# Optimization experiments

Hardware: AMD Instinct MI355X
Metric: run time of the kernel (lower is better)

## Reference

```python
import jax, jax.numpy as jnp
import numpy as np
from jax import lax

SK_ITERS = 32  # fixed number of morphological thinning steps (covers structures up to ~64px thick)


def _pool(x, op, init):
    # 3x3 'square' structuring element over [B, H, W]
    return lax.reduce_window(x, init, op, (1, 3, 3), (1, 1, 1), 'SAME')


def dilate(x):
    return _pool(x, lax.max, -jnp.inf)


def erode(x):
    return _pool(x, lax.min, jnp.inf)


def skeletonize(a):
    # Lantuejoul morphological skeleton with fixed iteration count (jit-friendly
    # stand-in for skimage Lee skeletonization + per-component CCL loop).
    # a: [B, H, W] binary float mask.
    def body(i, carry):
        e, s = carry
        opened = dilate(erode(e))
        s = jnp.maximum(s, e - opened)
        return erode(e), s

    _, s = lax.fori_loop(0, SK_ITERS, body, (a, jnp.zeros_like(a)))
    return s


def setup_inputs() -> dict:
    key = jax.random.key(0)
    k1, k2 = jax.random.split(key)
    pred = jax.random.normal(k1, (16, 2, 1024, 1024), dtype=jnp.float32)
    target = jax.random.randint(k2, (16, 1, 1024, 1024), 0, 2, dtype=jnp.int64)
    return {"pred": pred, "target": target, "epoch_num": 10}


def reference(pred, target, epoch_num):
    tgt = target[:, 0]                      # [B, H, W] int
    a = tgt.astype(pred.dtype)              # binary mask
    B, H, W = a.shape

    # foreground skeleton + dilated background skeleton (calc_back_skelen)
    fore_sk = skeletonize(a)
    back_sk = dilate(skeletonize(1.0 - a))

    # epoch-gated skeleton-aware pixel weight map (SkeletonAwareWeight)
    factor = jnp.minimum(jnp.asarray(epoch_num, pred.dtype) / 50.0, 1.0)
    w_map = 1.0 + factor * (fore_sk + back_sk)   # [B, H, W]

    # per-sample class weights: counts / min(counts); cw = sum(cw) - cw
    counts = jnp.stack([(tgt == 0).sum(axis=(1, 2)),
                        (tgt == 1).sum(axis=(1, 2))], axis=1).astype(pred.dtype)  # [B, 2]
    cw = counts / jnp.min(counts, axis=1, keepdims=True)
    cw = jnp.sum(cw, axis=1, keepdims=True) - cw                                   # [B, 2]
    cw_map = jnp.take_along_axis(cw, tgt.reshape(B, -1), axis=1).reshape(B, H, W)

    # weighted cross-entropy (WeightMapBortLoss core)
    logp = jax.nn.log_softmax(pred, axis=1)                       # [B, 2, H, W]
    ce = -jnp.take_along_axis(logp, tgt[:, None], axis=1)[:, 0]   # [B, H, W]
    return jnp.mean(w_map * cw_map * ce)
```

## Files before the change

### kernel.cpp

```cpp
#include <hip/hip_runtime.h>
#include <stdint.h>

typedef unsigned long long u64;
typedef unsigned int u32;
typedef unsigned short u16;

#define WPR 16
#define WORDS_PER_IMG (1024*WPR)
#define PIXELS_PER_IMG (1024*1024)
#define HALO 33
#define OWN 64
#define BROWS (OWN + 2*HALO)

__global__ __launch_bounds__(256) void k_pack(const int* __restrict__ tgt,
                                              u64* __restrict__ bits,
                                              u32* __restrict__ cpart) {
    __shared__ u16 marr[256];
    __shared__ u32 ws_[4];
    int t = threadIdx.x;
    const int4* p4 = (const int4*)(tgt + ((size_t)blockIdx.x * 256 + t) * 16);
    u32 m16 = 0;
    #pragma unroll
    for (int k = 0; k < 4; ++k) {
        int4 v = p4[k];
        m16 |= (u32)(v.x & 1) << (4 * k + 0);
        m16 |= (u32)(v.y & 1) << (4 * k + 1);
        m16 |= (u32)(v.z & 1) << (4 * k + 2);
        m16 |= (u32)(v.w & 1) << (4 * k + 3);
    }
    marr[t] = (u16)m16;
    u32 cnt = __popc(m16);
    for (int off = 32; off; off >>= 1) cnt += __shfl_down(cnt, off, 64);
    if ((t & 63) == 0) ws_[t >> 6] = cnt;
    __syncthreads();
    if (t < 64)
        bits[(size_t)blockIdx.x * 64 + t] = ((const u64*)marr)[t];
    if (t == 0) cpart[blockIdx.x] = ws_[0] + ws_[1] + ws_[2] + ws_[3];
}

__global__ __launch_bounds__(256) void k_skel(const u64* __restrict__ bits,
                                              u64* __restrict__ fore,
                                              u64* __restrict__ back) {
    __shared__ u64 bufs[3][BROWS][WPR];
    __shared__ int nz;
    int bid   = blockIdx.x;
    int strip = bid & 15;
    int task  = bid >> 4;
    int batch = task >> 1;
    int pol   = task & 1;
    int r0    = strip * OWN - HALO;
    const u64* img = bits + batch * WORDS_PER_IMG;

    u64 (*E)[WPR]  = bufs[0];
    u64 (*T1)[WPR] = bufs[1];
    u64 (*T2)[WPR] = bufs[2];

    int t = threadIdx.x;
    for (int idx = t; idx < BROWS * WPR; idx += 256) {
        int br = idx >> 4, w = idx & 15;
        int y = r0 + br;
        u64 v;
        if ((unsigned)y < 1024u) { v = img[(y << 4) + w]; if (pol) v = ~v; }
        else v = ~0ull;
        E[br][w] = v;
    }
    u64 s0 = 0, s1 = 0, s2 = 0, s3 = 0;
    __syncthreads();

    for (int k = 0; k < 32; ++k) {
        if (t == 0) nz = 0;
        for (int idx = t; idx < BROWS * WPR; idx += 256) {
            int br = idx >> 4, w = idx & 15;
            u64 c = E[br][w];
            u64 l = w ? E[br][w - 1] : ~0ull;
            u64 r = (w < 15) ? E[br][w + 1] : ~0ull;
            T1[br][w] = c & ((c << 1) | (l >> 63)) & ((c >> 1) | (r << 63));
        }
        __syncthreads();
        u64 anyv = 0;
        for (int idx = t; idx < BROWS * WPR; idx += 256) {
            int br = idx >> 4, w = idx & 15;
            int y  = r0 + br;
            u64 v = 0;
            if ((unsigned)y < 1024u) {
                u64 a_ = (br > 0 && (unsigned)(y - 1) < 1024u) ? T1[br - 1][w] : ~0ull;
                u64 b_ = T1[br][w];
                u64 c_ = (br < BROWS - 1 && (unsigned)(y + 1) < 1024u) ? T1[br + 1][w] : ~0ull;
                v = a_ & b_ & c_;
            }
            T2[br][w] = v;
            anyv |= v;
        }
        {
            u64 bal = __ballot(anyv != 0);
            if (bal && (t & 63) == 0) atomicOr(&nz, 1);
        }
        __syncthreads();
        if (nz == 0) {
            #pragma unroll
            for (int j = 0; j < 4; ++j) {
                int idx = t + j * 256;
                int br = HALO + (idx >> 4), w = idx & 15;
                u64 e = E[br][w];
                if (j == 0) s0 |= e; else if (j == 1) s1 |= e;
                else if (j == 2) s2 |= e; else s3 |= e;
            }
            break;
        }
        for (int idx = t; idx < BROWS * WPR; idx += 256) {
            int br = idx >> 4, w = idx & 15;
            u64 c = T2[br][w];
            u64 l = w ? T2[br][w - 1] : 0ull;
            u64 r = (w < 15) ? T2[br][w + 1] : 0ull;
            T1[br][w] = c | (c << 1) | (l >> 63) | (c >> 1) | (r << 63);
        }
        __syncthreads();
        #pragma unroll
        for (int j = 0; j < 4; ++j) {
            int idx = t + j * 256;
            int br = HALO + (idx >> 4), w = idx & 15;
            int y  = r0 + br;
            u64 a_ = ((unsigned)(y - 1) < 1024u) ? T1[br - 1][w] : 0ull;
            u64 b_ = T1[br][w];
            u64 c_ = ((unsigned)(y + 1) < 1024u) ? T1[br + 1][w] : 0ull;
            u64 add = E[br][w] & ~(a_ | b_ | c_);
            if (j == 0) s0 |= add; else if (j == 1) s1 |= add;
            else if (j == 2) s2 |= add; else s3 |= add;
        }
        u64 (*tmp)[WPR] = E; E = T2; T2 = tmp;
        __syncthreads();
    }

    u64* plane = (pol ? back : fore) + batch * WORDS_PER_IMG;
    #pragma unroll
    for (int j = 0; j < 4; ++j) {
        int idx = t + j * 256;
        int yo = strip * OWN + (idx >> 4);
        int w  = idx & 15;
        u64 sv = (j == 0) ? s0 : (j == 1) ? s1 : (j == 2) ? s2 : s3;
        plane[(yo << 4) + w] = sv;
    }
}

__global__ __launch_bounds__(256) void k_loss(const float* __restrict__ pred,
                                              const u64* __restrict__ bits,
                                              const u64* __restrict__ fore,
                                              const u64* __restrict__ back,
                                              const u32* __restrict__ cpart,
                                              const int* __restrict__ epochp,
                                              float* __restrict__ partials) {
    const float LOG2E = 1.4426950408889634f;
    const float LN2   = 0.6931471805599453f;

    int b = blockIdx.x >> 9;

    __shared__ u32 cs[4];
    __shared__ float s_c1;
    {
        u32 v = cpart[(b << 8) + threadIdx.x];
        for (int off = 32; off; off >>= 1) v += __shfl_down(v, off, 64);
        if ((threadIdx.x & 63) == 0) cs[threadIdx.x >> 6] = v;
        __syncthreads();
        if (threadIdx.x == 0) s_c1 = (float)(cs[0] + cs[1] + cs[2] + cs[3]);
        __syncthreads();
    }

    int tid = blockIdx.x * 256 + threadIdx.x;
    int p   = tid << 3;
    int rem = p & (PIXELS_PER_IMG - 1);
    int y   = rem >> 10;
    int x   = rem & 1023;

    const float* pb = pred + (size_t)b * (2 * PIXELS_PER_IMG);
    const float* r0p = pb + (y << 10) + x;
    const float* r1p = pb + PIXELS_PER_IMG + (y << 10) + x;
    float4 q0a = *(const float4*)(r0p);
    float4 q0b = *(const float4*)(r0p + 4);
    float4 q1a = *(const float4*)(r1p);
    float4 q1b = *(const float4*)(r1p + 4);

    int w  = x >> 6;
    int wi = (b << 14) + (y << 4) + w;
    u64 tw = bits[wi];
    u64 fw = fore[wi];

    const u64* bb = back + (b << 14);
    int rbase = y << 4;
    u64 m0 = bb[rbase + w];
    u64 mL = w ? bb[rbase + w - 1] : 0ull;
    u64 mR = (w < 15) ? bb[rbase + w + 1] : 0ull;
    if (y > 0) {
        m0 |= bb[rbase - 16 + w];
        if (w) mL |= bb[rbase - 16 + w - 1];
        if (w < 15) mR |= bb[rbase - 16 + w + 1];
    }
    if (y < 1023) {
        m0 |= bb[rbase + 16 + w];
        if (w) mL |= bb[rbase + 16 + w - 1];
        if (w < 15) mR |= bb[rbase + 16 + w + 1];
    }
    u64 dil = m0 | (m0 << 1) | (mL >> 63) | (m0 >> 1) | (mR << 63);

    float c1 = s_c1;
    float c0 = (float)PIXELS_PER_IMG - c1;
    float mn = fminf(c0, c1);
    float rmn = __builtin_amdgcn_rcpf(mn);
    float w0 = c1 * rmn, w1 = c0 * rmn;
    float factor = fminf((float)epochp[0] / 50.0f, 1.0f);

    int j0 = x & 63;
    u32 t8 = (u32)(tw  >> j0) & 255u;
    u32 f8 = (u32)(fw  >> j0) & 255u;
    u32 b8 = (u32)(dil >> j0) & 255u;

    float p0v[8] = {q0a.x, q0a.y, q0a.z, q0a.w, q0b.x, q0b.y, q0b.z, q0b.w};
    float p1v[8] = {q1a.x, q1a.y, q1a.z, q1a.w, q1b.x, q1b.y, q1b.z, q1b.w};

    float acc = 0.f;
    #pragma unroll
    for (int i = 0; i < 8; ++i) {
        u32 tt = (t8 >> i) & 1u;
        float fb = (float)(((f8 >> i) & 1u) + ((b8 >> i) & 1u));
        float wmap = 1.0f + factor * fb;
        float cw = tt ? w1 : w0;
        float diff  = p1v[i] - p0v[i];
        float adiff = fabsf(diff);
        float T = LN2 * __builtin_amdgcn_logf(1.0f + __builtin_amdgcn_exp2f(-adiff * LOG2E));
        float ce = fmaf(tt ? -0.5f : 0.5f, diff, fmaf(0.5f, adiff, T));
        acc = fmaf(wmap * cw, ce, acc);
    }
    for (int off = 32; off; off >>= 1) acc += __shfl_down(acc, off, 64);
    __shared__ float wsum[4];
    if ((threadIdx.x & 63) == 0) wsum[threadIdx.x >> 6] = acc;
    __syncthreads();
    if (threadIdx.x == 0)
        partials[blockIdx.x] = wsum[0] + wsum[1] + wsum[2] + wsum[3];
}

__global__ __launch_bounds__(256) void k_reduce(const float* __restrict__ partials,
                                                float* __restrict__ out) {
    double acc = 0.0;
    for (int i = threadIdx.x; i < 8192; i += 256) acc += (double)partials[i];
    for (int off = 32; off; off >>= 1) acc += __shfl_down(acc, off, 64);
    __shared__ double sd[4];
    if ((threadIdx.x & 63) == 0) sd[threadIdx.x >> 6] = acc;
    __syncthreads();
    if (threadIdx.x == 0)
        out[0] = (float)((sd[0] + sd[1] + sd[2] + sd[3]) / 16777216.0);
}

extern "C" void kernel_launch(void* const* d_in, const int* in_sizes, int n_in,
                              void* d_out, int out_size, void* d_ws, size_t ws_size,
                              hipStream_t stream) {
    const float* pred   = (const float*)d_in[0];
    const int*   target = (const int*)d_in[1];
    const int*   epoch  = (const int*)d_in[2];

    char* ws = (char*)d_ws;
    u32*   cpart    = (u32*)(ws + 1024);
    float* partials = (float*)(ws + (1u << 17));
    u64*   bits     = (u64*)(ws + (1u << 20));
    u64*   fore     = (u64*)(ws + (3u << 20));
    u64*   back     = (u64*)(ws + (5u << 20));

    hipLaunchKernelGGL(k_pack,   dim3(4096), dim3(256), 0, stream, target, bits, cpart);
    hipLaunchKernelGGL(k_skel,   dim3(512),  dim3(256), 0, stream, bits, fore, back);
    hipLaunchKernelGGL(k_loss,   dim3(8192), dim3(256), 0, stream, pred, bits, fore, back,
                       cpart, epoch, partials);
    hipLaunchKernelGGL(k_reduce, dim3(1),    dim3(256), 0, stream, partials, (float*)d_out);
}
```

Baseline: 66.21 us.

## Register-window fused erosion in skeleton kernel and shared-memory bit staging in loss

The skeleton kernel now maps one row-half (8 words) to each thread and computes the full 3x3 erosion and the opening's dilation from three-row register windows. The separate horizontal and vertical shared-memory passes are gone, which cuts each iteration to two buffers and two barriers, with a padded row stride. Strips are re-cut to 66 owned rows with a 31-row halo. The loss kernel loads each block's two rows of target, fore and back bit-words into shared memory and computes the back dilation once per word instead of once per thread. The reduced halo and the new strip geometry carry a boundary-correctness risk.

After: 58.40 us. 1.13x faster.

```diff
diff --git a/kernel.cpp b/kernel.cpp
--- a/kernel.cpp
+++ b/kernel.cpp
@@ -8,9 +8,11 @@
 #define WPR 16
 #define WORDS_PER_IMG (1024*WPR)
 #define PIXELS_PER_IMG (1024*1024)
-#define HALO 33
-#define OWN 64
-#define BROWS (OWN + 2*HALO)
+
+#define SOWN 66
+#define SHALO 31
+#define SROWS 128
+#define SPAD 17
 
 __global__ __launch_bounds__(256) void k_pack(const int* __restrict__ tgt,
                                               u64* __restrict__ bits,
@@ -41,105 +43,108 @@
 __global__ __launch_bounds__(256) void k_skel(const u64* __restrict__ bits,
                                               u64* __restrict__ fore,
                                               u64* __restrict__ back) {
-    __shared__ u64 bufs[3][BROWS][WPR];
-    __shared__ int nz;
+    __shared__ u64 bufA[SROWS][SPAD];
+    __shared__ u64 bufB[SROWS][SPAD];
+    __shared__ int nzbuf[2];
+
     int bid   = blockIdx.x;
     int strip = bid & 15;
     int task  = bid >> 4;
     int batch = task >> 1;
     int pol   = task & 1;
-    int r0    = strip * OWN - HALO;
+    int r0    = strip * SOWN - SHALO;
     const u64* img = bits + batch * WORDS_PER_IMG;
 
-    u64 (*E)[WPR]  = bufs[0];
-    u64 (*T1)[WPR] = bufs[1];
-    u64 (*T2)[WPR] = bufs[2];
-
-    int t = threadIdx.x;
-    for (int idx = t; idx < BROWS * WPR; idx += 256) {
-        int br = idx >> 4, w = idx & 15;
-        int y = r0 + br;
-        u64 v;
-        if ((unsigned)y < 1024u) { v = img[(y << 4) + w]; if (pol) v = ~v; }
-        else v = ~0ull;
-        E[br][w] = v;
-    }
-    u64 s0 = 0, s1 = 0, s2 = 0, s3 = 0;
-    __syncthreads();
-
-    for (int k = 0; k < 32; ++k) {
-        if (t == 0) nz = 0;
-        for (int idx = t; idx < BROWS * WPR; idx += 256) {
-            int br = idx >> 4, w = idx & 15;
-            u64 c = E[br][w];
-            u64 l = w ? E[br][w - 1] : ~0ull;
-            u64 r = (w < 15) ? E[br][w + 1] : ~0ull;
-            T1[br][w] = c & ((c << 1) | (l >> 63)) & ((c >> 1) | (r << 63));
-        }
+    int t  = threadIdx.x;
+    int r  = t >> 1;
+    int h  = t & 1;
+    int w0 = h << 3;
+    int y  = r0 + r;
+    bool yok   = ((unsigned)y < 1024u);
+    bool owned = yok && (r >= SHALO) && (r < SHALO + SOWN);
+
+    u64 (*E)[SPAD]  = bufA;
+    u64 (*Er)[SPAD] = bufB;
+
+    if (yok) {
+        const u64* src = img + (y << 4) + w0;
+        #pragma unroll
+        for (int k = 0; k < 8; ++k) {
+            u64 v = src[k];
+            E[r][w0 + k] = pol ? ~v : v;
+        }
+    } else {
+        #pragma unroll
+        for (int k = 0; k < 8; ++k) E[r][w0 + k] = 0;
+    }
+    if (t < 2) nzbuf[t] = 0;
+
+    u64 s[8] = {0,0,0,0,0,0,0,0};
+    u64 corig[8];
+
+    auto ldwin = [&](u64 (*B)[SPAD], int rr, u64 oob, u64* d) {
+        int yy = r0 + rr;
+        if (rr >= 0 && rr < SROWS && (unsigned)yy < 1024u) {
+            d[0] = (w0 > 0) ? B[rr][w0 - 1] : oob;
+            #pragma unroll
+            for (int k = 0; k < 8; ++k) d[k + 1] = B[rr][w0 + k];
+            d[9] = (w0 + 8 < 16) ? B[rr][w0 + 8] : oob;
+        } else {
+            #pragma unroll
+            for (int k = 0; k < 10; ++k) d[k] = oob;
+        }
+    };
+    #define HOR_E(d, k) (d[k] & ((d[k] << 1) | (d[k-1] >> 63)) & ((d[k] >> 1) | (d[k+1] << 63)))
+    #define HOR_D(d, k) (d[k] | (d[k] << 1) | (d[k-1] >> 63) | (d[k] >> 1) | (d[k+1] << 63))
+
+    __syncthreads();
+    for (int it = 0; it < 32; ++it) {
+        u64 rm[10], rc[10], rp[10];
+        ldwin(E, r - 1, ~0ull, rm);
+        ldwin(E, r,     ~0ull, rc);
+        ldwin(E, r + 1, ~0ull, rp);
+        u64 any = 0;
+        #pragma unroll
+        for (int k = 0; k < 8; ++k) {
+            u64 v = HOR_E(rm, k + 1) & HOR_E(rc, k + 1) & HOR_E(rp, k + 1);
+            if (!yok) v = 0;
+            any |= v;
+            corig[k] = rc[k + 1];
+            Er[r][w0 + k] = v;
+        }
+        u64 bal = __ballot(any != 0);
+        if (bal && (t & 63) == 0) atomicOr(&nzbuf[it & 1], 1);
+        if (t == 0) nzbuf[(it + 1) & 1] = 0;
         __syncthreads();
-        u64 anyv = 0;
-        for (int idx = t; idx < BROWS * WPR; idx += 256) {
-            int br = idx >> 4, w = idx & 15;
-            int y  = r0 + br;
-            u64 v = 0;
-            if ((unsigned)y < 1024u) {
-                u64 a_ = (br > 0 && (unsigned)(y - 1) < 1024u) ? T1[br - 1][w] : ~0ull;
-                u64 b_ = T1[br][w];
-                u64 c_ = (br < BROWS - 1 && (unsigned)(y + 1) < 1024u) ? T1[br + 1][w] : ~0ull;
-                v = a_ & b_ & c_;
-            }
-            T2[br][w] = v;
-            anyv |= v;
-        }
-        {
-            u64 bal = __ballot(anyv != 0);
-            if (bal && (t & 63) == 0) atomicOr(&nz, 1);
-        }
-        __syncthreads();
-        if (nz == 0) {
-            #pragma unroll
-            for (int j = 0; j < 4; ++j) {
-                int idx = t + j * 256;
-                int br = HALO + (idx >> 4), w = idx & 15;
-                u64 e = E[br][w];
-                if (j == 0) s0 |= e; else if (j == 1) s1 |= e;
-                else if (j == 2) s2 |= e; else s3 |= e;
+        if (nzbuf[it & 1] == 0) {
+            if (owned) {
+                #pragma unroll
+                for (int k = 0; k < 8; ++k) s[k] |= corig[k];
             }
             break;
         }
-        for (int idx = t; idx < BROWS * WPR; idx += 256) {
-            int br = idx >> 4, w = idx & 15;
-            u64 c = T2[br][w];
-            u64 l = w ? T2[br][w - 1] : 0ull;
-            u64 r = (w < 15) ? T2[br][w + 1] : 0ull;
-            T1[br][w] = c | (c << 1) | (l >> 63) | (c >> 1) | (r << 63);
-        }
+        if (owned) {
+            u64 dm[10], dc[10], dp[10];
+            ldwin(Er, r - 1, 0ull, dm);
+            ldwin(Er, r,     0ull, dc);
+            ldwin(Er, r + 1, 0ull, dp);
+            #pragma unroll
+            for (int k = 0; k < 8; ++k) {
+                u64 op = HOR_D(dm, k + 1) | HOR_D(dc, k + 1) | HOR_D(dp, k + 1);
+                s[k] |= corig[k] & ~op;
+            }
+        }
+        { u64 (*tmp)[SPAD] = E; E = Er; Er = tmp; }
         __syncthreads();
-        #pragma unroll
-        for (int j = 0; j < 4; ++j) {
-            int idx = t + j * 256;
-            int br = HALO + (idx >> 4), w = idx & 15;
-            int y  = r0 + br;
-            u64 a_ = ((unsigned)(y - 1) < 1024u) ? T1[br - 1][w] : 0ull;
-            u64 b_ = T1[br][w];
-            u64 c_ = ((unsigned)(y + 1) < 1024u) ? T1[br + 1][w] : 0ull;
-            u64 add = E[br][w] & ~(a_ | b_ | c_);
-            if (j == 0) s0 |= add; else if (j == 1) s1 |= add;
-            else if (j == 2) s2 |= add; else s3 |= add;
-        }
-        u64 (*tmp)[WPR] = E; E = T2; T2 = tmp;
-        __syncthreads();
-    }
-
-    u64* plane = (pol ? back : fore) + batch * WORDS_PER_IMG;
-    #pragma unroll
-    for (int j = 0; j < 4; ++j) {
-        int idx = t + j * 256;
-        int yo = strip * OWN + (idx >> 4);
-        int w  = idx & 15;
-        u64 sv = (j == 0) ? s0 : (j == 1) ? s1 : (j == 2) ? s2 : s3;
-        plane[(yo << 4) + w] = sv;
-    }
+    }
+
+    if (owned) {
+        u64* plane = (pol ? back : fore) + batch * WORDS_PER_IMG + (y << 4) + w0;
+        #pragma unroll
+        for (int k = 0; k < 8; ++k) plane[k] = s[k];
+    }
+    #undef HOR_E
+    #undef HOR_D
 }
 
 __global__ __launch_bounds__(256) void k_loss(const float* __restrict__ pred,
@@ -152,26 +157,50 @@
     const float LOG2E = 1.4426950408889634f;
     const float LN2   = 0.6931471805599453f;
 
-    int b = blockIdx.x >> 9;
-
+    __shared__ u64 tb[2][16], tf[2][16], tbk[4][16], dil[2][16];
     __shared__ u32 cs[4];
     __shared__ float s_c1;
-    {
-        u32 v = cpart[(b << 8) + threadIdx.x];
-        for (int off = 32; off; off >>= 1) v += __shfl_down(v, off, 64);
-        if ((threadIdx.x & 63) == 0) cs[threadIdx.x >> 6] = v;
-        __syncthreads();
-        if (threadIdx.x == 0) s_c1 = (float)(cs[0] + cs[1] + cs[2] + cs[3]);
-        __syncthreads();
-    }
-
-    int tid = blockIdx.x * 256 + threadIdx.x;
-    int p   = tid << 3;
-    int rem = p & (PIXELS_PER_IMG - 1);
-    int y   = rem >> 10;
-    int x   = rem & 1023;
-
-    const float* pb = pred + (size_t)b * (2 * PIXELS_PER_IMG);
+    __shared__ float wsum[4];
+
+    int bid = blockIdx.x;
+    int b   = bid >> 9;
+    int rp  = bid & 511;
+    int y0  = rp << 1;
+    int t   = threadIdx.x;
+
+    u32 v = cpart[(b << 8) + t];
+    for (int off = 32; off; off >>= 1) v += __shfl_down(v, off, 64);
+    if ((t & 63) == 0) cs[t >> 6] = v;
+
+    int base = b << 14;
+    if (t < 32) {
+        int i = t >> 4, w = t & 15;
+        tb[i][w] = bits[base + ((y0 + i) << 4) + w];
+    } else if (t < 64) {
+        int tt = t - 32; int i = tt >> 4, w = tt & 15;
+        tf[i][w] = fore[base + ((y0 + i) << 4) + w];
+    } else if (t < 128) {
+        int tt = t - 64; int i = tt >> 4, w = tt & 15;
+        int yy = y0 - 1 + i;
+        tbk[i][w] = ((unsigned)yy < 1024u) ? back[base + (yy << 4) + w] : 0ull;
+    }
+    __syncthreads();
+    if (t < 32) {
+        int i = t >> 4, w = t & 15;
+        u64 m0 = tbk[i][w] | tbk[i + 1][w] | tbk[i + 2][w];
+        u64 mL = (w > 0)  ? (tbk[i][w - 1] | tbk[i + 1][w - 1] | tbk[i + 2][w - 1]) : 0ull;
+        u64 mR = (w < 15) ? (tbk[i][w + 1] | tbk[i + 1][w + 1] | tbk[i + 2][w + 1]) : 0ull;
+        dil[i][w] = m0 | (m0 << 1) | (mL >> 63) | (m0 >> 1) | (mR << 63);
+    }
+    if (t == 0) s_c1 = (float)(cs[0] + cs[1] + cs[2] + cs[3]);
+    __syncthreads();
+
+    int ry = t >> 7;
+    int xq = t & 127;
+    int x  = xq << 3;
+    int y  = y0 + ry;
+
+    const float* pb  = pred + (size_t)b * (2 * PIXELS_PER_IMG);
     const float* r0p = pb + (y << 10) + x;
     const float* r1p = pb + PIXELS_PER_IMG + (y << 10) + x;
     float4 q0a = *(const float4*)(r0p);
@@ -179,27 +208,10 @@
     float4 q1a = *(const float4*)(r1p);
     float4 q1b = *(const float4*)(r1p + 4);
 
-    int w  = x >> 6;
-    int wi = (b << 14) + (y << 4) + w;
-    u64 tw = bits[wi];
-    u64 fw = fore[wi];
-
-    const u64* bb = back + (b << 14);
-    int rbase = y << 4;
-    u64 m0 = bb[rbase + w];
-    u64 mL = w ? bb[rbase + w - 1] : 0ull;
-    u64 mR = (w < 15) ? bb[rbase + w + 1] : 0ull;
-    if (y > 0) {
-        m0 |= bb[rbase - 16 + w];
-        if (w) mL |= bb[rbase - 16 + w - 1];
-        if (w < 15) mR |= bb[rbase - 16 + w + 1];
-    }
-    if (y < 1023) {
-        m0 |= bb[rbase + 16 + w];
-        if (w) mL |= bb[rbase + 16 + w - 1];
-        if (w < 15) mR |= bb[rbase + 16 + w + 1];
-    }
-    u64 dil = m0 | (m0 << 1) | (mL >> 63) | (m0 >> 1) | (mR << 63);
+    int wq = xq >> 3;
+    u64 tw = tb[ry][wq];
+    u64 fw = tf[ry][wq];
+    u64 dl = dil[ry][wq];
 
     float c1 = s_c1;
     float c0 = (float)PIXELS_PER_IMG - c1;
@@ -208,10 +220,10 @@
     float w0 = c1 * rmn, w1 = c0 * rmn;
     float factor = fminf((float)epochp[0] / 50.0f, 1.0f);
 
-    int j0 = x & 63;
-    u32 t8 = (u32)(tw  >> j0) & 255u;
-    u32 f8 = (u32)(fw  >> j0) & 255u;
-    u32 b8 = (u32)(dil >> j0) & 255u;
+    int j0 = (t & 7) << 3;
+    u32 t8 = (u32)(tw >> j0) & 255u;
+    u32 f8 = (u32)(fw >> j0) & 255u;
+    u32 b8 = (u32)(dl >> j0) & 255u;
 
     float p0v[8] = {q0a.x, q0a.y, q0a.z, q0a.w, q0b.x, q0b.y, q0b.z, q0b.w};
     float p1v[8] = {q1a.x, q1a.y, q1a.z, q1a.w, q1b.x, q1b.y, q1b.z, q1b.w};
@@ -230,11 +242,10 @@
         acc = fmaf(wmap * cw, ce, acc);
     }
     for (int off = 32; off; off >>= 1) acc += __shfl_down(acc, off, 64);
-    __shared__ float wsum[4];
-    if ((threadIdx.x & 63) == 0) wsum[threadIdx.x >> 6] = acc;
-    __syncthreads();
-    if (threadIdx.x == 0)
-        partials[blockIdx.x] = wsum[0] + wsum[1] + wsum[2] + wsum[3];
+    if ((t & 63) == 0) wsum[t >> 6] = acc;
+    __syncthreads();
+    if (t == 0)
+        partials[bid] = wsum[0] + wsum[1] + wsum[2] + wsum[3];
 }
 
 __global__ __launch_bounds__(256) void k_reduce(const float* __restrict__ partials,
```
